# Kernel optimization log

Hardware: AMD Instinct MI355X
Metric: run time of the kernel (lower is better)

The kernel has to match this reference:

```python
import jax, jax.numpy as jnp
import numpy as np

S, B, E = 1024, 2, 1024   # seq, batch, emsize
H = 16                    # nheads
HD = E // H               # head dim
D_FF = 4096               # nhid
N_EXP = 8                 # num experts (world_size=1 -> all local)
EPS = 1e-5


def setup_inputs() -> dict:
    key = jax.random.key(0)
    ks = jax.random.split(key, 12)
    s = 0.02
    return {
        "x": jax.random.normal(ks[0], (S, B, E), jnp.float32),
        "in_proj_w": jax.random.normal(ks[1], (3 * E, E), jnp.float32) * s,
        "in_proj_b": jnp.zeros((3 * E,), jnp.float32),
        "out_proj_w": jax.random.normal(ks[2], (E, E), jnp.float32) * s,
        "out_proj_b": jnp.zeros((E,), jnp.float32),
        "ln1_g": jnp.ones((E,), jnp.float32),
        "ln1_b": jnp.zeros((E,), jnp.float32),
        "ln2_g": jnp.ones((E,), jnp.float32),
        "ln2_b": jnp.zeros((E,), jnp.float32),
        "gate_w": jax.random.normal(ks[3], (N_EXP, E), jnp.float32) * s,
        "gate_b": jnp.zeros((N_EXP,), jnp.float32),
        "w1": jax.random.normal(ks[4], (N_EXP, D_FF, E), jnp.float32) * s,
        "b1": jnp.zeros((N_EXP, D_FF), jnp.float32),
        "w2": jax.random.normal(ks[5], (N_EXP, E, D_FF), jnp.float32) * s,
        "b2": jnp.zeros((N_EXP, E), jnp.float32),
    }


def _layernorm(x, g, b):
    mu = jnp.mean(x, axis=-1, keepdims=True)
    var = jnp.var(x, axis=-1, keepdims=True)
    return (x - mu) * jax.lax.rsqrt(var + EPS) * g + b


def _mha(x, in_proj_w, in_proj_b, out_proj_w, out_proj_b):
    # x: [S, B, E] (torch MultiheadAttention default layout)
    qkv = x @ in_proj_w.T + in_proj_b                # [S, B, 3E]
    q, k, v = jnp.split(qkv, 3, axis=-1)
    q = q.reshape(S, B, H, HD) * (1.0 / np.sqrt(HD))
    k = k.reshape(S, B, H, HD)
    v = v.reshape(S, B, H, HD)
    scores = jnp.einsum("sbhd,tbhd->bhst", q, k)     # [B, H, S, S]
    attn = jax.nn.softmax(scores, axis=-1)
    o = jnp.einsum("bhst,tbhd->sbhd", attn, v).reshape(S, B, E)
    return o @ out_proj_w.T + out_proj_b


def _moe(x, gate_w, gate_b, w1, b1, w2, b2):
    # top-1 routing (fmoe NaiveGate, top_k=1 -> combine weight is exactly 1.0)
    t = x.reshape(S * B, E)
    logits = t @ gate_w.T + gate_b                   # [T, N_EXP]
    eid = jnp.argmax(logits, axis=-1)                # [T]
    out = jnp.zeros_like(t)
    for e in range(N_EXP):                           # fixed small expert loop
        h = jax.nn.gelu(t @ w1[e].T + b1[e], approximate=False) @ w2[e].T + b2[e]
        out = out + jnp.where((eid == e)[:, None], h, 0.0)
    return out.reshape(S, B, E)


def reference(x, in_proj_w, in_proj_b, out_proj_w, out_proj_b,
              ln1_g, ln1_b, ln2_g, ln2_b,
              gate_w, gate_b, w1, b1, w2, b2):
    x = _layernorm(x + _mha(x, in_proj_w, in_proj_b, out_proj_w, out_proj_b), ln1_g, ln1_b)
    x = _layernorm(x + _moe(x, gate_w, gate_b, w1, b1, w2, b2), ln2_g, ln2_b)
    return x
```

## Files before the change

kernel.cpp:

```cpp
#include <hip/hip_runtime.h>
#include <hip/hip_bf16.h>
#include <math.h>

#define DI __device__ __forceinline__

typedef __bf16 bf16_t;
typedef bf16_t bf16x8 __attribute__((ext_vector_type(8)));
typedef bf16_t bf16x4 __attribute__((ext_vector_type(4)));
typedef float f32x4 __attribute__((ext_vector_type(4)));

constexpr int S_ = 1024, B_ = 2, E_ = 1024, H_ = 16, HD_ = 64;
constexpr int T_ = S_ * B_;
constexpr int DFF_ = 4096, NE_ = 8;
constexpr int SLOTS_ = 3072;
constexpr int SPLITK_ = 4;

DI f32x4 mfma16(bf16x8 a, bf16x8 b, f32x4 c) {
  return __builtin_amdgcn_mfma_f32_16x16x32_bf16(a, b, c, 0, 0, 0);
}

DI void split2(float v, bf16_t& h, bf16_t& l) {
  h = (bf16_t)v;
  l = (bf16_t)(v - (float)h);
}

typedef const __attribute__((address_space(1))) void* gas_p;
typedef __attribute__((address_space(3))) void* las_p;
DI void gll16(const void* g, void* l) {
  __builtin_amdgcn_global_load_lds((gas_p)g, (las_p)l, 16, 0, 0);
}

DI int swslot(int u, int r) { return u ^ (r & 7); }

template <int NCH, int LOG2NCH>
DI void prep_w_load(const float* src, int f, f32x4& a, f32x4& b) {
  int u = f & 7, chunk = (f >> 3) & (NCH - 1), row = f >> (3 + LOG2NCH);
  const float* s = src + (size_t)row * (NCH * 64) + chunk * 64 + u * 8;
  a = *(const f32x4*)s;
  b = *(const f32x4*)(s + 4);
}
template <int NCH, int LOG2NCH>
DI void prep_w_store(bf16_t* dst, int f, f32x4 a, f32x4 b) {
  int u = f & 7, chunk = (f >> 3) & (NCH - 1), row = f >> (3 + LOG2NCH);
  bf16x8 o;
#pragma unroll
  for (int j = 0; j < 4; j++) { o[j] = (bf16_t)a[j]; o[4 + j] = (bf16_t)b[j]; }
  char* d = (char*)dst + (size_t)row * (NCH * 128) + chunk * 128 + swslot(u, row) * 16;
  *(bf16x8*)d = o;
}

DI void do_prep_wsplit(const float* src, bf16_t* dst, int f) {
  int u = f & 3, chunk = (f >> 2) & 31, row = f >> 7;
  const float* s = src + (size_t)row * 1024 + chunk * 32 + u * 8;
  f32x4 a = *(const f32x4*)s, b = *(const f32x4*)(s + 4);
  bf16x8 hv, lv;
#pragma unroll
  for (int j = 0; j < 4; j++) {
    bf16_t h, l; split2(a[j], h, l); hv[j] = h; lv[j] = l;
    split2(b[j], h, l); hv[4 + j] = h; lv[4 + j] = l;
  }
  char* base = (char*)dst + (size_t)row * 4096 + chunk * 128;
  *(bf16x8*)(base + swslot(u, row) * 16) = hv;
  *(bf16x8*)(base + swslot(u + 4, row) * 16) = lv;
}

__launch_bounds__(256)
__global__ void prep_all(const float* ipw, bf16_t* ipwp,
                         const float* opw, bf16_t* opwp,
                         const float* x, bf16_t* xp, int* cnt) {
  int b = blockIdx.x, tid = threadIdx.x;
  if (b < 1536) {
    do_prep_wsplit(ipw, ipwp, b * 256 + tid);
  } else if (b < 2048) {
    do_prep_wsplit(opw, opwp, (b - 1536) * 256 + tid);
  } else if (b < 3072) {
    do_prep_wsplit(x, xp, (b - 2048) * 256 + tid);
  } else {
    if (tid < 8) cnt[tid] = 0;
  }
}

template <int MODE>
__launch_bounds__(256, 2)
__global__ void gemm_kernel(const bf16_t* Ap, const bf16_t* Bp0,
                            const float* bias,
                            float* Cf, bf16_t* Cb,
                            bf16_t* Qh, bf16_t* Ql, bf16_t* Kh2, bf16_t* Kl2,
                            bf16_t* Vh2, bf16_t* Vl2,
                            const int* offs_pad,
                            const float* W2f, bf16_t* W2p) {
  constexpr bool SPLIT = (MODE <= 1);
  constexpr int NK = (MODE == 0) ? 32 : 16;
  constexpr int ARB = (MODE == 2) ? 2048 : ((MODE == 3) ? 8192 : 4096);
  constexpr int BUFB = 32768;
  extern __shared__ char smem[];

  const int tid = threadIdx.x, lane = tid & 63, wv = tid >> 6;
  int n0, m0;
  if constexpr (MODE == 2) {
    int b = blockIdx.x;
    if (b >= 768) {
      int bu = (b - 768) * 8;
      f32x4 va[8], vb[8];
#pragma unroll
      for (int it = 0; it < 8; it++)
        prep_w_load<64, 6>(W2f, (bu + it) * 256 + tid, va[it], vb[it]);
#pragma unroll
      for (int it = 0; it < 8; it++)
        prep_w_store<64, 6>(W2p, (bu + it) * 256 + tid, va[it], vb[it]);
      return;
    }
    n0 = (b & 31) * 128;
    m0 = (b >> 5) * 128;
  } else {
    n0 = blockIdx.x * 128;
    m0 = blockIdx.y * 128;
  }

  int e = 0;
  if constexpr (MODE >= 2) {
    if (m0 >= offs_pad[8]) return;
#pragma unroll
    for (int i = 1; i < 8; i++) e += (m0 >= offs_pad[i]);
  }
  const int kz = (MODE == 1 || MODE == 3) ? blockIdx.z : 0;
  const int ck0 = (MODE == 1 || MODE == 3) ? kz * 16 : 0;

  const char* Ab = (const char*)Ap;
  const char* Bb = (const char*)Bp0;
  if constexpr (MODE == 2) Bb += (size_t)e * 4096 * 2048;
  if constexpr (MODE == 3) Bb += (size_t)e * 1024 * 8192;

  auto STAGE = [&](char* lb, int ck) {
#pragma unroll
    for (int i = 0; i < 4; i++) {
      int f = i * 256 + tid, row = f >> 3, cb = (f & 7) * 16;
      gll16(Ab + (size_t)(m0 + row) * ARB + ck * 128 + cb, lb + f * 16);
    }
#pragma unroll
    for (int i = 0; i < 4; i++) {
      int f = i * 256 + tid, row = f >> 3, cb = (f & 7) * 16;
      gll16(Bb + (size_t)(n0 + row) * ARB + ck * 128 + cb, lb + 16384 + f * 16);
    }
  };

  f32x4 acc[4][4];
#pragma unroll
  for (int i = 0; i < 4; i++)
#pragma unroll
    for (int j = 0; j < 4; j++) acc[i][j] = (f32x4){0.f, 0.f, 0.f, 0.f};

  const int wm = (wv >> 1) * 64, wn = (wv & 1) * 64;
  const int lr = lane & 15;

  auto LB = [&](const char* base, int r, int u) {
    return *(const bf16x8*)(base + r * 128 + (swslot(u, r) << 4));
  };
  auto COMPUTE = [&](const char* lb) {
    const char* Abase = lb;
    const char* Bbase = lb + 16384;
    if constexpr (SPLIT) {
      const int u = lane >> 4;
      bf16x8 afh[4], afl[4];
#pragma unroll
      for (int fm = 0; fm < 4; fm++) {
        int r = wm + fm * 16 + lr;
        afh[fm] = LB(Abase, r, u);
        afl[fm] = LB(Abase, r, u + 4);
      }
#pragma unroll
      for (int fn = 0; fn < 4; fn++) {
        int r = wn + fn * 16 + lr;
        bf16x8 bfh = LB(Bbase, r, u);
        bf16x8 bfl = LB(Bbase, r, u + 4);
#pragma unroll
        for (int fm = 0; fm < 4; fm++) {
          acc[fm][fn] = mfma16(afh[fm], bfh, acc[fm][fn]);
          acc[fm][fn] = mfma16(afh[fm], bfl, acc[fm][fn]);
          acc[fm][fn] = mfma16(afl[fm], bfh, acc[fm][fn]);
        }
      }
    } else {
#pragma unroll
      for (int kk = 0; kk < 2; kk++) {
        const int u = kk * 4 + (lane >> 4);
        bf16x8 af[4];
#pragma unroll
        for (int fm = 0; fm < 4; fm++) af[fm] = LB(Abase, wm + fm * 16 + lr, u);
#pragma unroll
        for (int fn = 0; fn < 4; fn++) {
          bf16x8 bf = LB(Bbase, wn + fn * 16 + lr, u);
#pragma unroll
          for (int fm = 0; fm < 4; fm++) acc[fm][fn] = mfma16(af[fm], bf, acc[fm][fn]);
        }
      }
    }
  };

  STAGE(smem, ck0);
  __syncthreads();
  int cur = 0;
  for (int kt = 0; kt < NK; ++kt) {
    if (kt + 1 < NK) STAGE(smem + (cur ^ 1) * BUFB, ck0 + kt + 1);
    COMPUTE(smem + cur * BUFB);
    __syncthreads();
    cur ^= 1;
  }

  const int lr4 = (lane >> 4) * 4;
#pragma unroll
  for (int fm = 0; fm < 4; fm++) {
#pragma unroll
    for (int fn = 0; fn < 4; fn++) {
#pragma unroll
      for (int r = 0; r < 4; r++) {
        float v = acc[fm][fn][r];
        int row = wm + fm * 16 + lr4 + r;
        int col = wn + fn * 16 + lr;
        if constexpr (MODE == 0) {
          int gm = m0 + row, gn = n0 + col;
          v += bias[gn];
          int sec = gn >> 10, ee = gn & 1023, hh = ee >> 6, dd = ee & 63;
          if (sec == 0) v *= 0.125f;
          int ss = gm >> 1, bb = gm & 1, bhp = bb * 16 + hh;
          size_t base = ((size_t)bhp * 1024 + ss) * 64;
          bf16_t oh, ol; split2(v, oh, ol);
          if (sec == 0) {
            Qh[base + dd] = oh; Ql[base + dd] = ol;
          } else {
            size_t di = base + ((size_t)swslot(dd >> 3, ss) << 3) + (dd & 7);
            bf16_t* dh = (sec == 1) ? Kh2 : Vh2;
            bf16_t* dl = (sec == 1) ? Kl2 : Vl2;
            dh[di] = oh; dl[di] = ol;
          }
        } else if constexpr (MODE == 1) {
          int gm = m0 + row, gn = n0 + col;
          Cf[((size_t)kz * T_ + gm) * E_ + gn] = v;
        } else if constexpr (MODE == 2) {
          int slot = m0 + row, gn = n0 + col;
          v += bias[e * DFF_ + gn];
          v = 0.5f * v * (1.0f + erff(v * 0.70710678118654752440f));
          size_t byte = (size_t)slot * 8192 + (gn >> 6) * 128 +
                        (swslot((gn & 63) >> 3, slot) << 4) + (gn & 7) * 2;
          *(bf16_t*)((char*)Cb + byte) = (bf16_t)v;
        } else {
          int slot = m0 + row, gn = n0 + col;
          Cb[((size_t)kz * SLOTS_ + slot) * E_ + gn] = (bf16_t)v;
        }
      }
    }
  }
}

__launch_bounds__(256)
__global__ void vtrans_kernel(const bf16_t* vh, const bf16_t* vl,
                              bf16_t* vth, bf16_t* vtl) {
  const int bh = blockIdx.y, s0 = blockIdx.x * 64;
  const int tid = threadIdx.x;
  __shared__ bf16_t th[64][72];
  __shared__ bf16_t tl[64][72];
#pragma unroll
  for (int i = 0; i < 2; i++) {
    int f = tid + i * 256, r = f >> 3, c = (f & 7) * 8;
    int s = s0 + r;
    size_t rowb = ((size_t)bh * 1024 + s) * 128;
    *(bf16x8*)&th[r][c] = *(const bf16x8*)((const char*)vh + rowb + (swslot(c >> 3, s) << 4));
    *(bf16x8*)&tl[r][c] = *(const bf16x8*)((const char*)vl + rowb + (swslot(c >> 3, s) << 4));
  }
  __syncthreads();
#pragma unroll
  for (int i = 0; i < 2; i++) {
    int f = tid + i * 256, d = f >> 3, c2 = (f & 7) * 8;
    bf16x8 oh, ol;
#pragma unroll
    for (int j = 0; j < 8; j++) { oh[j] = th[c2 + j][d]; ol[j] = tl[c2 + j][d]; }
    size_t ob = (((size_t)bh * 64 + d) * 1024 + s0) * 2;
    *(bf16x8*)((char*)vth + ob + (swslot(c2 >> 3, d) << 4)) = oh;
    *(bf16x8*)((char*)vtl + ob + (swslot(c2 >> 3, d) << 4)) = ol;
  }
}

__launch_bounds__(256)
__global__ void attn_kernel(const bf16_t* gqh, const bf16_t* gql,
                            const bf16_t* gkh, const bf16_t* gkl,
                            const bf16_t* gvth, const bf16_t* gvtl,
                            bf16_t* ao,
                            const float* W1f, bf16_t* W1p) {
  const int tid = threadIdx.x, lane = tid & 63, wv = tid >> 6;
  {
    int b = blockIdx.x;
    if (b >= 512) {
      int bu = (b - 512) * 8;
      f32x4 va[8], vb[8];
#pragma unroll
      for (int it = 0; it < 8; it++)
        prep_w_load<16, 4>(W1f, (bu + it) * 256 + tid, va[it], vb[it]);
#pragma unroll
      for (int it = 0; it < 8; it++)
        prep_w_store<16, 4>(W1p, (bu + it) * 256 + tid, va[it], vb[it]);
      return;
    }
  }
  const int bh = blockIdx.x >> 4, q0 = (blockIdx.x & 15) * 64;
  const int lr = lane & 15, lk = (lane >> 4) * 8, lr4 = (lane >> 4) * 4;
  extern __shared__ char smem[];
  char* Kh = smem;
  char* Kl = smem + 8192;
  char* Vh = smem + 16384;
  char* Vl = smem + 24576;
  char* Ph = smem + 32768;
  char* Pl = smem + 40960;

  const size_t qbase = ((size_t)bh * 1024 + q0 + wv * 16 + lr) * 64;
  bf16x8 qfh[2], qfl[2];
  qfh[0] = *(const bf16x8*)&gqh[qbase + lk];
  qfh[1] = *(const bf16x8*)&gqh[qbase + 32 + lk];
  qfl[0] = *(const bf16x8*)&gql[qbase + lk];
  qfl[1] = *(const bf16x8*)&gql[qbase + 32 + lk];

  f32x4 oacc[4];
#pragma unroll
  for (int i = 0; i < 4; i++) oacc[i] = (f32x4){0.f, 0.f, 0.f, 0.f};
  float m_r[4], l_r[4];
#pragma unroll
  for (int r = 0; r < 4; r++) { m_r[r] = -INFINITY; l_r[r] = 0.f; }

  for (int t0 = 0; t0 < S_; t0 += 64) {
    __syncthreads();
#pragma unroll
    for (int i = 0; i < 2; i++) {
      int f = i * 256 + tid, row = f >> 3, cb = (f & 7) * 16;
      size_t koff = ((size_t)bh * 1024 + t0 + row) * 128 + cb;
      gll16((const char*)gkh + koff, Kh + f * 16);
      gll16((const char*)gkl + koff, Kl + f * 16);
      size_t voff = (((size_t)bh * 64 + row) * 1024 + t0) * 2 + cb;
      gll16((const char*)gvth + voff, Vh + f * 16);
      gll16((const char*)gvtl + voff, Vl + f * 16);
    }
    __syncthreads();

    f32x4 sacc[4];
#pragma unroll
    for (int i = 0; i < 4; i++) sacc[i] = (f32x4){0.f, 0.f, 0.f, 0.f};
#pragma unroll
    for (int kk = 0; kk < 2; ++kk) {
      const int u = kk * 4 + (lane >> 4);
#pragma unroll
      for (int fn = 0; fn < 4; ++fn) {
        int r = fn * 16 + lr;
        bf16x8 kbh = *(const bf16x8*)(Kh + r * 128 + (swslot(u, r) << 4));
        bf16x8 kbl = *(const bf16x8*)(Kl + r * 128 + (swslot(u, r) << 4));
        sacc[fn] = mfma16(qfh[kk], kbh, sacc[fn]);
        sacc[fn] = mfma16(qfh[kk], kbl, sacc[fn]);
        sacc[fn] = mfma16(qfl[kk], kbh, sacc[fn]);
      }
    }
#pragma unroll
    for (int r = 0; r < 4; r++) {
      float mx = fmaxf(fmaxf(sacc[0][r], sacc[1][r]), fmaxf(sacc[2][r], sacc[3][r]));
#pragma unroll
      for (int off = 1; off < 16; off <<= 1) mx = fmaxf(mx, __shfl_xor(mx, off));
      float mn = m_r[r];
      if (mx > mn) {
        mn = mx;
        float al = __expf(m_r[r] - mn);
        l_r[r] *= al;
#pragma unroll
        for (int fd = 0; fd < 4; fd++) oacc[fd][r] *= al;
        m_r[r] = mn;
      }
      float ps = 0.f;
      int pr = wv * 16 + lr4 + r;
#pragma unroll
      for (int fn = 0; fn < 4; fn++) {
        float p = __expf(sacc[fn][r] - mn);
        ps += p;
        bf16_t ph, pl; split2(p, ph, pl);
        int colu = (fn * 16 + lr) >> 3;
        int byte = pr * 128 + (swslot(colu, pr) << 4) + ((lr & 7) * 2);
        *(bf16_t*)(Ph + byte) = ph;
        *(bf16_t*)(Pl + byte) = pl;
      }
#pragma unroll
      for (int off = 1; off < 16; off <<= 1) ps += __shfl_xor(ps, off);
      l_r[r] += ps;
    }
#pragma unroll
    for (int kk = 0; kk < 2; kk++) {
      const int u = kk * 4 + (lane >> 4);
      int pr2 = wv * 16 + lr;
      bf16x8 pah = *(const bf16x8*)(Ph + pr2 * 128 + (swslot(u, pr2) << 4));
      bf16x8 pal = *(const bf16x8*)(Pl + pr2 * 128 + (swslot(u, pr2) << 4));
#pragma unroll
      for (int fd = 0; fd < 4; fd++) {
        int rd = fd * 16 + lr;
        bf16x8 vbh = *(const bf16x8*)(Vh + rd * 128 + (swslot(u, rd) << 4));
        bf16x8 vbl = *(const bf16x8*)(Vl + rd * 128 + (swslot(u, rd) << 4));
        oacc[fd] = mfma16(pah, vbh, oacc[fd]);
        oacc[fd] = mfma16(pah, vbl, oacc[fd]);
        oacc[fd] = mfma16(pal, vbh, oacc[fd]);
      }
    }
  }
  const int b = bh >> 4, h = bh & 15;
#pragma unroll
  for (int fd = 0; fd < 4; fd++) {
#pragma unroll
    for (int r = 0; r < 4; r++) {
      float v = oacc[fd][r] / l_r[r];
      int s = q0 + wv * 16 + lr4 + r;
      int d = fd * 16 + lr;
      int tok = s * 2 + b;
      int chunk = h * 2 + (d >> 5);
      int w = d & 31;
      bf16_t oh, ol; split2(v, oh, ol);
      size_t rb = (size_t)tok * 4096 + chunk * 128;
      *(bf16_t*)((char*)ao + rb + (swslot(w >> 3, tok) << 4) + (w & 7) * 2) = oh;
      *(bf16_t*)((char*)ao + rb + (swslot(4 + (w >> 3), tok) << 4) + (w & 7) * 2) = ol;
    }
  }
}

__launch_bounds__(256)
__global__ void ln1gate_kernel(const float* p0, const float* p1, const float* x,
                               const float* opb, const float* g, const float* bt,
                               const float* gw, const float* gb,
                               float* l1f, int* eid, int* cnt) {
  const int row = blockIdx.x, tid = threadIdx.x;
  const int j = tid * 4;
  f32x4 v = *(const f32x4*)&p0[(size_t)row * 1024 + j];
  f32x4 v1 = *(const f32x4*)&p1[(size_t)row * 1024 + j];
  f32x4 xr = *(const f32x4*)&x[(size_t)row * 1024 + j];
  f32x4 bb2 = *(const f32x4*)&opb[j];
#pragma unroll
  for (int i = 0; i < 4; i++) v[i] += v1[i] + xr[i] + bb2[i];
  float s = v[0] + v[1] + v[2] + v[3];
  float q = v[0] * v[0] + v[1] * v[1] + v[2] * v[2] + v[3] * v[3];
#pragma unroll
  for (int off = 1; off < 64; off <<= 1) { s += __shfl_xor(s, off); q += __shfl_xor(q, off); }
  __shared__ float ss[4], qq[4];
  __shared__ float gp[4][8];
  int wv = tid >> 6;
  if ((tid & 63) == 0) { ss[wv] = s; qq[wv] = q; }
  __syncthreads();
  s = ss[0] + ss[1] + ss[2] + ss[3];
  q = qq[0] + qq[1] + qq[2] + qq[3];
  float mu = s * (1.f / 1024.f);
  float var = q * (1.f / 1024.f) - mu * mu;
  float rs = rsqrtf(var + 1e-5f);
  f32x4 gg = *(const f32x4*)&g[j];
  f32x4 bb = *(const f32x4*)&bt[j];
  f32x4 o;
#pragma unroll
  for (int jj = 0; jj < 4; jj++) o[jj] = (v[jj] - mu) * rs * gg[jj] + bb[jj];
  *(f32x4*)&l1f[(size_t)row * 1024 + j] = o;

  float a[8];
#pragma unroll
  for (int ee = 0; ee < 8; ee++) {
    f32x4 wv4 = *(const f32x4*)&gw[ee * 1024 + j];
    a[ee] = o[0] * wv4[0] + o[1] * wv4[1] + o[2] * wv4[2] + o[3] * wv4[3];
  }
#pragma unroll
  for (int ee = 0; ee < 8; ee++)
#pragma unroll
    for (int off = 1; off < 64; off <<= 1) a[ee] += __shfl_xor(a[ee], off);
  if ((tid & 63) == 0) {
#pragma unroll
    for (int ee = 0; ee < 8; ee++) gp[wv][ee] = a[ee];
  }
  __syncthreads();
  if (tid == 0) {
    float best = -1e30f;
    int be = 0;
#pragma unroll
    for (int ee = 0; ee < 8; ee++) {
      float vv = gp[0][ee] + gp[1][ee] + gp[2][ee] + gp[3][ee] + gb[ee];
      if (vv > best) { best = vv; be = ee; }
    }
    eid[row] = be;
    atomicAdd(&cnt[be], 1);
  }
}

__launch_bounds__(256)
__global__ void ln2_kernel(const bf16_t* part, const float* l1f, const float* b2,
                           const int* eid, const int* inv, const float* g,
                           const float* bt, float* out) {
  const int t = blockIdx.x, tid = threadIdx.x;
  const int st = inv[t], e = eid[t];
  const int j = tid * 4;
  f32x4 v = (f32x4){0.f, 0.f, 0.f, 0.f};
#pragma unroll
  for (int kz = 0; kz < SPLITK_; kz++) {
    bf16x4 p = *(const bf16x4*)&part[((size_t)kz * SLOTS_ + st) * 1024 + j];
#pragma unroll
    for (int i = 0; i < 4; i++) v[i] += (float)p[i];
  }
  f32x4 bb2 = *(const f32x4*)&b2[e * 1024 + j];
  f32x4 rr = *(const f32x4*)&l1f[(size_t)t * 1024 + j];
#pragma unroll
  for (int i = 0; i < 4; i++) v[i] += bb2[i] + rr[i];
  float s = v[0] + v[1] + v[2] + v[3];
  float q = v[0] * v[0] + v[1] * v[1] + v[2] * v[2] + v[3] * v[3];
#pragma unroll
  for (int off = 1; off < 64; off <<= 1) { s += __shfl_xor(s, off); q += __shfl_xor(q, off); }
  __shared__ float ss[4], qq[4];
  int wv = tid >> 6;
  if ((tid & 63) == 0) { ss[wv] = s; qq[wv] = q; }
  __syncthreads();
  s = ss[0] + ss[1] + ss[2] + ss[3];
  q = qq[0] + qq[1] + qq[2] + qq[3];
  float mu = s * (1.f / 1024.f);
  float var = q * (1.f / 1024.f) - mu * mu;
  float rs = rsqrtf(var + 1e-5f);
  f32x4 gg = *(const f32x4*)&g[j];
  f32x4 bb = *(const f32x4*)&bt[j];
  f32x4 o;
#pragma unroll
  for (int jj = 0; jj < 4; jj++) o[jj] = (v[jj] - mu) * rs * gg[jj] + bb[jj];
  *(f32x4*)&out[(size_t)t * 1024 + j] = o;
}

__global__ void scan_kernel(const int* cnt, int* offs_pad, int* cur) {
  if (threadIdx.x == 0) {
    int op = 0;
    for (int e = 0; e < 8; e++) {
      offs_pad[e] = op;
      op += (cnt[e] + 127) & ~127;
      cur[e] = 0;
    }
    offs_pad[8] = op;
  }
}

__launch_bounds__(256)
__global__ void scatter_gather(const int* eid, const int* offs_pad, int* cur,
                               int* inv, const float* l1f, bf16_t* l1g) {
  const int t = blockIdx.x * 4 + (threadIdx.x >> 6);
  const int lane = threadIdx.x & 63;
  int slot = 0;
  if (lane == 0) {
    int ee = eid[t];
    int pos = atomicAdd(&cur[ee], 1);
    slot = offs_pad[ee] + pos;
    inv[t] = slot;
  }
  slot = __shfl(slot, 0);
#pragma unroll
  for (int i = 0; i < 2; i++) {
    int chunk = (lane >> 3) + i * 8, u = lane & 7;
    const float* s = l1f + (size_t)t * 1024 + chunk * 64 + u * 8;
    f32x4 a = *(const f32x4*)s, b = *(const f32x4*)(s + 4);
    bf16x8 o;
#pragma unroll
    for (int j = 0; j < 4; j++) { o[j] = (bf16_t)a[j]; o[4 + j] = (bf16_t)b[j]; }
    char* d = (char*)l1g + (size_t)slot * 2048 + chunk * 128 + swslot(u, slot) * 16;
    *(bf16x8*)d = o;
  }
}

extern "C" void kernel_launch(void* const* d_in, const int* in_sizes, int n_in,
                              void* d_out, int out_size, void* d_ws, size_t ws_size,
                              hipStream_t stream) {
  const float* x    = (const float*)d_in[0];
  const float* ipw  = (const float*)d_in[1];
  const float* ipb  = (const float*)d_in[2];
  const float* opw  = (const float*)d_in[3];
  const float* opb  = (const float*)d_in[4];
  const float* ln1g = (const float*)d_in[5];
  const float* ln1b = (const float*)d_in[6];
  const float* ln2g = (const float*)d_in[7];
  const float* ln2b = (const float*)d_in[8];
  const float* gw   = (const float*)d_in[9];
  const float* gb   = (const float*)d_in[10];
  const float* w1   = (const float*)d_in[11];
  const float* b1   = (const float*)d_in[12];
  const float* w2   = (const float*)d_in[13];
  const float* b2   = (const float*)d_in[14];
  float* out = (float*)d_out;

  char* w = (char*)d_ws;
  auto alloc = [&](size_t n) { char* p = w; w += (n + 255) & ~(size_t)255; return p; };
  const size_t MB = 1u << 20;

  char* R1 = alloc(64 * MB);
  bf16_t* w1p   = (bf16_t*)R1;
  bf16_t* partb = (bf16_t*)R1;
  bf16_t* w2p = (bf16_t*)alloc(64 * MB);
  char* R3 = alloc(8 * MB);
  bf16_t* xp  = (bf16_t*)R3;
  bf16_t* l1g = (bf16_t*)R3;
  bf16_t* ipwp = (bf16_t*)alloc(12 * MB);
  bf16_t* opwp = (bf16_t*)alloc(4 * MB);
  char* R6 = alloc(32 * MB);
  bf16_t* qh  = (bf16_t*)(R6 + 0 * MB);
  bf16_t* ql  = (bf16_t*)(R6 + 4 * MB);
  bf16_t* kh  = (bf16_t*)(R6 + 8 * MB);
  bf16_t* kl  = (bf16_t*)(R6 + 12 * MB);
  bf16_t* vh  = (bf16_t*)(R6 + 16 * MB);
  bf16_t* vl  = (bf16_t*)(R6 + 20 * MB);
  bf16_t* vth = (bf16_t*)(R6 + 24 * MB);
  bf16_t* vtl = (bf16_t*)(R6 + 28 * MB);
  bf16_t* hbuf = (bf16_t*)R6;
  bf16_t* ao    = (bf16_t*)alloc(8 * MB);
  float*  pre1p = (float*)alloc(16 * MB);
  float*  l1f   = (float*)alloc(8 * MB);
  int* eid   = (int*)alloc(T_ * 4);
  int* cnt   = (int*)alloc(16 * 4);
  int* offsp = (int*)alloc(16 * 4);
  int* cur   = (int*)alloc(16 * 4);
  int* inv   = (int*)alloc(T_ * 4);

  const dim3 blk(256);
  const int smemGemm = 65536;
  const int smemAttn = 49152;

  prep_all<<<dim3(3073), blk, 0, stream>>>(ipw, ipwp, opw, opwp, x, xp, cnt);

  gemm_kernel<0><<<dim3(24, 16), blk, smemGemm, stream>>>(
      xp, ipwp, ipb, nullptr, nullptr,
      qh, ql, kh, kl, vh, vl, nullptr, nullptr, nullptr);

  vtrans_kernel<<<dim3(16, 32), blk, 0, stream>>>(vh, vl, vth, vtl);

  attn_kernel<<<dim3(2560), blk, smemAttn, stream>>>(qh, ql, kh, kl, vth, vtl,
                                                     ao, w1, w1p);

  gemm_kernel<1><<<dim3(8, 16, 2), blk, smemGemm, stream>>>(
      ao, opwp, nullptr, pre1p, nullptr,
      nullptr, nullptr, nullptr, nullptr, nullptr, nullptr, nullptr,
      nullptr, nullptr);

  ln1gate_kernel<<<dim3(T_), blk, 0, stream>>>(pre1p, pre1p + (size_t)T_ * E_, x,
                                               opb, ln1g, ln1b, gw, gb,
                                               l1f, eid, cnt);

  scan_kernel<<<1, 64, 0, stream>>>(cnt, offsp, cur);
  scatter_gather<<<dim3(T_ / 4), blk, 0, stream>>>(eid, offsp, cur, inv, l1f, l1g);

  gemm_kernel<2><<<dim3(2816), blk, smemGemm, stream>>>(
      l1g, w1p, b1, nullptr, hbuf,
      nullptr, nullptr, nullptr, nullptr, nullptr, nullptr, offsp,
      w2, w2p);

  gemm_kernel<3><<<dim3(8, 24, SPLITK_), blk, smemGemm, stream>>>(
      hbuf, w2p, nullptr, nullptr, partb,
      nullptr, nullptr, nullptr, nullptr, nullptr, nullptr, offsp,
      nullptr, nullptr);

  ln2_kernel<<<dim3(T_), blk, 0, stream>>>(partb, l1f, b2, eid, inv, ln2g, ln2b, out);

  (void)in_sizes; (void)n_in; (void)out_size; (void)ws_size;
}
```

Before: 334.2 us.

## Move W2 weight packing into QKV and out-proj GEMMs; exp2 softmax with MFMA row sums

The W2 bf16 hi/lo packing work is moved out of the expert-FFN1 GEMM launch and split across extra blocks in the QKV projection and out-projection GEMM launches. Those launches underfill the GPU, so the packing can run alongside their tiles and the critical-path FFN1 launch shrinks. Attention now folds log2(e) into the Q scale and uses exp2f, and computes softmax row sums with an MFMA against a ones vector instead of shuffle reductions. This trades a few extra MFMAs for fewer shuffles.

```diff
diff --git a/kernel.cpp b/kernel.cpp
--- a/kernel.cpp
+++ b/kernel.cpp
@@ -96,11 +96,11 @@
   extern __shared__ char smem[];
 
   const int tid = threadIdx.x, lane = tid & 63, wv = tid >> 6;
-  int n0, m0;
-  if constexpr (MODE == 2) {
+  int n0, m0, kz = 0;
+  if constexpr (MODE == 0) {
     int b = blockIdx.x;
-    if (b >= 768) {
-      int bu = (b - 768) * 8;
+    if (b >= 384) {
+      int bu = (b - 384) * 8;
       f32x4 va[8], vb[8];
 #pragma unroll
       for (int it = 0; it < 8; it++)
@@ -110,11 +110,28 @@
         prep_w_store<64, 6>(W2p, (bu + it) * 256 + tid, va[it], vb[it]);
       return;
     }
-    n0 = (b & 31) * 128;
-    m0 = (b >> 5) * 128;
+    n0 = (b % 24) * 128;
+    m0 = (b / 24) * 128;
+  } else if constexpr (MODE == 1) {
+    int b = blockIdx.x;
+    if (b >= 256) {
+      int bu = 8192 + (b - 256) * 8;
+      f32x4 va[8], vb[8];
+#pragma unroll
+      for (int it = 0; it < 8; it++)
+        prep_w_load<64, 6>(W2f, (bu + it) * 256 + tid, va[it], vb[it]);
+#pragma unroll
+      for (int it = 0; it < 8; it++)
+        prep_w_store<64, 6>(W2p, (bu + it) * 256 + tid, va[it], vb[it]);
+      return;
+    }
+    n0 = (b & 7) * 128;
+    m0 = ((b >> 3) & 15) * 128;
+    kz = b >> 7;
   } else {
     n0 = blockIdx.x * 128;
     m0 = blockIdx.y * 128;
+    if constexpr (MODE == 3) kz = blockIdx.z;
   }
 
   int e = 0;
@@ -123,7 +140,6 @@
 #pragma unroll
     for (int i = 1; i < 8; i++) e += (m0 >= offs_pad[i]);
   }
-  const int kz = (MODE == 1 || MODE == 3) ? blockIdx.z : 0;
   const int ck0 = (MODE == 1 || MODE == 3) ? kz * 16 : 0;
 
   const char* Ab = (const char*)Ap;
@@ -221,7 +237,7 @@
           int gm = m0 + row, gn = n0 + col;
           v += bias[gn];
           int sec = gn >> 10, ee = gn & 1023, hh = ee >> 6, dd = ee & 63;
-          if (sec == 0) v *= 0.125f;
+          if (sec == 0) v *= 0.18033688011112042f;
           int ss = gm >> 1, bb = gm & 1, bhp = bb * 16 + hh;
           size_t base = ((size_t)bhp * 1024 + ss) * 64;
           bf16_t oh, ol; split2(v, oh, ol);
@@ -318,12 +334,17 @@
   qfl[0] = *(const bf16x8*)&gql[qbase + lk];
   qfl[1] = *(const bf16x8*)&gql[qbase + 32 + lk];
 
+  bf16x8 ones8;
+#pragma unroll
+  for (int i = 0; i < 8; i++) ones8[i] = (bf16_t)1.0f;
+
   f32x4 oacc[4];
 #pragma unroll
   for (int i = 0; i < 4; i++) oacc[i] = (f32x4){0.f, 0.f, 0.f, 0.f};
-  float m_r[4], l_r[4];
-#pragma unroll
-  for (int r = 0; r < 4; r++) { m_r[r] = -INFINITY; l_r[r] = 0.f; }
+  f32x4 lacc = (f32x4){0.f, 0.f, 0.f, 0.f};
+  float m_r[4];
+#pragma unroll
+  for (int r = 0; r < 4; r++) m_r[r] = -INFINITY;
 
   for (int t0 = 0; t0 < S_; t0 += 64) {
     __syncthreads();
@@ -360,30 +381,23 @@
       float mx = fmaxf(fmaxf(sacc[0][r], sacc[1][r]), fmaxf(sacc[2][r], sacc[3][r]));
 #pragma unroll
       for (int off = 1; off < 16; off <<= 1) mx = fmaxf(mx, __shfl_xor(mx, off));
-      float mn = m_r[r];
-      if (mx > mn) {
-        mn = mx;
-        float al = __expf(m_r[r] - mn);
-        l_r[r] *= al;
+      if (mx > m_r[r]) {
+        float al = exp2f(m_r[r] - mx);
+        lacc[r] *= al;
 #pragma unroll
         for (int fd = 0; fd < 4; fd++) oacc[fd][r] *= al;
-        m_r[r] = mn;
-      }
-      float ps = 0.f;
+        m_r[r] = mx;
+      }
       int pr = wv * 16 + lr4 + r;
 #pragma unroll
       for (int fn = 0; fn < 4; fn++) {
-        float p = __expf(sacc[fn][r] - mn);
-        ps += p;
+        float p = exp2f(sacc[fn][r] - m_r[r]);
         bf16_t ph, pl; split2(p, ph, pl);
         int colu = (fn * 16 + lr) >> 3;
         int byte = pr * 128 + (swslot(colu, pr) << 4) + ((lr & 7) * 2);
         *(bf16_t*)(Ph + byte) = ph;
         *(bf16_t*)(Pl + byte) = pl;
       }
-#pragma unroll
-      for (int off = 1; off < 16; off <<= 1) ps += __shfl_xor(ps, off);
-      l_r[r] += ps;
     }
 #pragma unroll
     for (int kk = 0; kk < 2; kk++) {
@@ -391,6 +405,8 @@
       int pr2 = wv * 16 + lr;
       bf16x8 pah = *(const bf16x8*)(Ph + pr2 * 128 + (swslot(u, pr2) << 4));
       bf16x8 pal = *(const bf16x8*)(Pl + pr2 * 128 + (swslot(u, pr2) << 4));
+      lacc = mfma16(pah, ones8, lacc);
+      lacc = mfma16(pal, ones8, lacc);
 #pragma unroll
       for (int fd = 0; fd < 4; fd++) {
         int rd = fd * 16 + lr;
@@ -407,7 +423,7 @@
   for (int fd = 0; fd < 4; fd++) {
 #pragma unroll
     for (int r = 0; r < 4; r++) {
-      float v = oacc[fd][r] / l_r[r];
+      float v = oacc[fd][r] / lacc[r];
       int s = q0 + wv * 16 + lr4 + r;
       int d = fd * 16 + lr;
       int tok = s * 2 + b;
@@ -618,19 +634,19 @@
 
   prep_all<<<dim3(3073), blk, 0, stream>>>(ipw, ipwp, opw, opwp, x, xp, cnt);
 
-  gemm_kernel<0><<<dim3(24, 16), blk, smemGemm, stream>>>(
+  gemm_kernel<0><<<dim3(1408), blk, smemGemm, stream>>>(
       xp, ipwp, ipb, nullptr, nullptr,
-      qh, ql, kh, kl, vh, vl, nullptr, nullptr, nullptr);
+      qh, ql, kh, kl, vh, vl, nullptr, w2, w2p);
 
   vtrans_kernel<<<dim3(16, 32), blk, 0, stream>>>(vh, vl, vth, vtl);
 
   attn_kernel<<<dim3(2560), blk, smemAttn, stream>>>(qh, ql, kh, kl, vth, vtl,
                                                      ao, w1, w1p);
 
-  gemm_kernel<1><<<dim3(8, 16, 2), blk, smemGemm, stream>>>(
+  gemm_kernel<1><<<dim3(1280), blk, smemGemm, stream>>>(
       ao, opwp, nullptr, pre1p, nullptr,
       nullptr, nullptr, nullptr, nullptr, nullptr, nullptr, nullptr,
-      nullptr, nullptr);
+      w2, w2p);
 
   ln1gate_kernel<<<dim3(T_), blk, 0, stream>>>(pre1p, pre1p + (size_t)T_ * E_, x,
                                                opb, ln1g, ln1b, gw, gb,
@@ -639,10 +655,10 @@
   scan_kernel<<<1, 64, 0, stream>>>(cnt, offsp, cur);
   scatter_gather<<<dim3(T_ / 4), blk, 0, stream>>>(eid, offsp, cur, inv, l1f, l1g);
 
-  gemm_kernel<2><<<dim3(2816), blk, smemGemm, stream>>>(
+  gemm_kernel<2><<<dim3(32, 24), blk, smemGemm, stream>>>(
       l1g, w1p, b1, nullptr, hbuf,
       nullptr, nullptr, nullptr, nullptr, nullptr, nullptr, offsp,
-      w2, w2p);
+      nullptr, nullptr);
 
   gemm_kernel<3><<<dim3(8, 24, SPLITK_), blk, smemGemm, stream>>>(
       hbuf, w2p, nullptr, nullptr, partb,
```

Measured after the change: 350.4 us. 4.8% more time.
